# Kernel tuning notes

Hardware: AMD Instinct MI355X
Metric: run time of the kernel (lower is better)

## Reference

```python
import jax, jax.numpy as jnp
import numpy as np

EPS = 1e-6


def setup_inputs() -> dict:
    key = jax.random.key(0)
    T, B, D, n, K = 2048, 16, 1024, 64, 3
    k0, k1, k2 = jax.random.split(key, 3)
    x = jax.random.normal(k0, (T, B, D), dtype=jnp.float32)
    # xavier-ish scale for projections
    scale = 1.0 / np.sqrt(D).astype(np.float32)
    W_kv = jax.random.normal(k1, (K * 2 * n, D), dtype=jnp.float32) * scale
    W_q = jax.random.normal(k2, (n, D), dtype=jnp.float32) * scale
    B_gates = jnp.full((K, n), 2.0, dtype=jnp.float32)  # init.constant_(B_gates, 2.0)
    M_init = jnp.zeros((K, B, n, n), dtype=jnp.float32)
    return {"x": x, "M_init": M_init, "W_kv": W_kv, "W_q": W_q, "B_gates": B_gates}


def reference(x, M_init, W_kv, W_q, B_gates):
    # x: [T, B, D]; M_init: [K, B, n, n]; W_kv: [K*2*n, D]; W_q: [n, D]; B_gates: [K, n]
    T, B, D = x.shape
    K, n = B_gates.shape
    # fused kv projection, interleaved per level: [T, B, K, 2, n]
    kv = jnp.einsum('tbd,pd->tbp', x, W_kv).reshape(T, B, K, 2, n)
    k_all = jnp.transpose(kv[:, :, :, 0, :], (0, 2, 1, 3))  # [T, K, B, n]
    v_all = jnp.transpose(kv[:, :, :, 1, :], (0, 2, 1, 3))  # [T, K, B, n]
    q_all = jnp.einsum('tbd,nd->tbn', x, W_q)                # [T, B, n]
    b = B_gates[:, None, :]                                  # [K, 1, n] broadcast over batch

    def step(M, inputs):
        # M: [K, B, n, n]
        k_t, v_t, q_t = inputs
        k_norm = k_t / (jnp.linalg.norm(k_t, axis=-1, keepdims=True) + EPS)  # [K,B,n]
        gater = jnp.roll(M, shift=-1, axis=0)  # gater for level i is M[(i+1) % K]
        row_gate = jax.nn.sigmoid(jnp.einsum('kbij,kbj->kbi', gater, k_norm) + b)
        col_gate = jax.nn.sigmoid(jnp.einsum('kbji,kbj->kbi', gater, k_norm) + b)
        retrieved = jnp.einsum('kbij,kbj->kbi', M, k_norm)
        delta = v_t - retrieved
        M_new = (row_gate[..., None] * M * col_gate[:, :, None, :]
                 + jnp.einsum('kbi,kbj->kbij', delta, k_norm))
        Sq = jnp.einsum('bij,bj->bi', M_new[0], q_t)  # query against tower 0
        out = Sq * jax.nn.sigmoid(Sq)                  # self-gated output (SiLU self-gate)
        return M_new, out

    M_final, outputs = jax.lax.scan(step, M_init, (k_all, v_all, q_all))
    return outputs, M_final  # [T, B, n], [K, B, n, n]
```

## Files before the change

kernel.cpp:

```cpp
#include <hip/hip_runtime.h>
#include <hip/hip_bf16.h>
#include <math.h>

#define TT 2048
#define BB_ 16
#define DD 1024
#define NN 64
#define KK 3
#define PP 448

typedef float  v2f  __attribute__((ext_vector_type(2)));
typedef float  f4   __attribute__((ext_vector_type(4)));
typedef float  f32x4 __attribute__((ext_vector_type(4)));
typedef short  bh8  __attribute__((ext_vector_type(8)));

__device__ __forceinline__ float sigmoidf_(float x) {
    return 1.0f / (1.0f + __expf(-x));
}

#define LDS_BARRIER() __asm__ volatile("s_waitcnt lgkmcnt(0)\n\ts_barrier" ::: "memory")

template<int CTRL>
__device__ __forceinline__ float dpp_mov(float v) {
    int r = __builtin_amdgcn_update_dpp(0, __float_as_int(v), CTRL, 0xF, 0xF, true);
    return __int_as_float(r);
}

__device__ __forceinline__ float sel16_dpp(const float v[4], int s) {
    const int s0 = s & 1, s1 = (s >> 1) & 1;
    float k0 = s0 ? v[1] : v[0], d0 = s0 ? v[0] : v[1];
    float k1 = s0 ? v[3] : v[2], d1 = s0 ? v[2] : v[3];
    float a0 = k0 + dpp_mov<0xB1>(d0);
    float a1 = k1 + dpp_mov<0xB1>(d1);
    float kb = s1 ? a1 : a0, db = s1 ? a0 : a1;
    float r  = kb + dpp_mov<0x4E>(db);
    r += dpp_mov<0x124>(r);
    r += dpp_mov<0x128>(r);
    return r;
}

__global__ __launch_bounds__(256) void cvt_w_kernel(
    const float* __restrict__ Wkv,
    const float* __restrict__ Wq,
    unsigned short* __restrict__ Wsw)
{
    const int n = blockIdx.x;
    const int tid = threadIdx.x;
    const float* row = (n < 384) ? (Wkv + (size_t)n * DD)
                                 : (Wq  + (size_t)(n - 384) * DD);
    const int idx = tid * 4;
    const int kb = idx >> 5, kk = idx & 31;
    float4 f = *(const float4*)(row + idx);
    __hip_bfloat162 h0 = __float22bfloat162_rn(make_float2(f.x, f.y));
    __hip_bfloat162 h1 = __float22bfloat162_rn(make_float2(f.z, f.w));
    unsigned u0, u1;
    __builtin_memcpy(&u0, &h0, 4);
    __builtin_memcpy(&u1, &h1, 4);
    ushort4 o = make_ushort4((unsigned short)u0, (unsigned short)(u0 >> 16),
                             (unsigned short)u1, (unsigned short)(u1 >> 16));
    *(ushort4*)&Wsw[((size_t)kb * PP + n) * 32 + kk] = o;
}

__global__ __launch_bounds__(256) void mfma_proj_kernel(
    const float* __restrict__ x,
    const unsigned short* __restrict__ Wsw,
    float* __restrict__ kvq)
{
    const int tid  = threadIdx.x;
    const int w    = tid >> 6;
    const int lane = tid & 63;
    const int ln   = lane & 15;
    const int quad = lane >> 4;
    const int m0   = blockIdx.x * 64;

    f32x4 acc[28];
    #pragma unroll
    for (int t = 0; t < 28; ++t) acc[t] = (f32x4){0.f, 0.f, 0.f, 0.f};

    const float* xrow = x + (size_t)(m0 + 16 * w + ln) * DD + quad * 8;

    for (int kb = 0; kb < 32; ++kb) {
        float4 a0 = *(const float4*)(xrow + kb * 32);
        float4 a1 = *(const float4*)(xrow + kb * 32 + 4);
        __hip_bfloat162 h0 = __float22bfloat162_rn(make_float2(a0.x, a0.y));
        __hip_bfloat162 h1 = __float22bfloat162_rn(make_float2(a0.z, a0.w));
        __hip_bfloat162 h2 = __float22bfloat162_rn(make_float2(a1.x, a1.y));
        __hip_bfloat162 h3 = __float22bfloat162_rn(make_float2(a1.z, a1.w));
        unsigned u0, u1, u2, u3;
        __builtin_memcpy(&u0, &h0, 4); __builtin_memcpy(&u1, &h1, 4);
        __builtin_memcpy(&u2, &h2, 4); __builtin_memcpy(&u3, &h3, 4);
        bh8 a;
        a[0] = (short)u0; a[1] = (short)(u0 >> 16);
        a[2] = (short)u1; a[3] = (short)(u1 >> 16);
        a[4] = (short)u2; a[5] = (short)(u2 >> 16);
        a[6] = (short)u3; a[7] = (short)(u3 >> 16);

        const unsigned short* wp_ = Wsw + (size_t)kb * PP * 32 + quad * 8;
        #pragma unroll
        for (int t = 0; t < 28; ++t) {
            const bh8 bfr = *(const bh8*)(wp_ + (16 * t + ln) * 32);
            acc[t] = __builtin_amdgcn_mfma_f32_16x16x32_bf16(a, bfr, acc[t], 0, 0, 0);
        }
    }

    #pragma unroll
    for (int g = 0; g < 3; ++g) {
        const int t0 = g * 8;
        #pragma unroll
        for (int reg = 0; reg < 4; ++reg) {
            float ss = acc[t0][reg] * acc[t0][reg]
                     + acc[t0 + 1][reg] * acc[t0 + 1][reg]
                     + acc[t0 + 2][reg] * acc[t0 + 2][reg]
                     + acc[t0 + 3][reg] * acc[t0 + 3][reg];
            #pragma unroll
            for (int m = 1; m <= 8; m <<= 1) ss += __shfl_xor(ss, m, 64);
            const float sc = 1.0f / (sqrtf(ss) + 1e-6f);
            #pragma unroll
            for (int t = t0; t < t0 + 4; ++t) acc[t][reg] *= sc;
        }
    }

    float* orow = kvq + (size_t)(m0 + 16 * w + quad * 4) * PP + ln;
    #pragma unroll
    for (int t = 0; t < 28; ++t)
        #pragma unroll
        for (int reg = 0; reg < 4; ++reg)
            orow[(size_t)reg * PP + 16 * t] = acc[t][reg];
}

__global__ __launch_bounds__(1024) void scan_kernel(
    const float* __restrict__ kvq,
    const float* __restrict__ M_init,
    const float* __restrict__ B_gates,
    float* __restrict__ d_out)
{
    const int b    = blockIdx.x;
    const int tid  = threadIdx.x;
    const int wid  = tid >> 6;
    const int lane = tid & 63;

    __shared__ __align__(16) float cs_lds[2][3][4][4][64];
    __shared__ __align__(16) float rg_lds[2][3][64];
    __shared__ __align__(16) float cg_lds[2][3][64];

    if (wid >= 12) {
        const int  act = (wid < 15);
        const int  cls = act ? (wid - 12) : 0;
        const float cbias = act ? B_gates[cls * NN + lane] : 0.f;
        #pragma unroll 2
        for (int t = 0; t < TT; ++t) {
            const int pb = t & 1;
            LDS_BARRIER();
            if (act) {
                float s0 = (cs_lds[pb][cls][0][0][lane] + cs_lds[pb][cls][0][1][lane])
                         + (cs_lds[pb][cls][0][2][lane] + cs_lds[pb][cls][0][3][lane]);
                float s1 = (cs_lds[pb][cls][1][0][lane] + cs_lds[pb][cls][1][1][lane])
                         + (cs_lds[pb][cls][1][2][lane] + cs_lds[pb][cls][1][3][lane]);
                float s2 = (cs_lds[pb][cls][2][0][lane] + cs_lds[pb][cls][2][1][lane])
                         + (cs_lds[pb][cls][2][2][lane] + cs_lds[pb][cls][2][3][lane]);
                float s3 = (cs_lds[pb][cls][3][0][lane] + cs_lds[pb][cls][3][1][lane])
                         + (cs_lds[pb][cls][3][2][lane] + cs_lds[pb][cls][3][3][lane]);
                cg_lds[pb][cls][lane] = sigmoidf_((s0 + s1) + (s2 + s3) + cbias);
            }
            LDS_BARRIER();
        }
        return;
    }

    const int k    = wid >> 2;
    const int q    = wid & 3;
    const int tr   = lane >> 4;
    const int tc   = lane & 15;
    const int kp   = (k + 2) % 3;
    const int row0 = 16 * q + 4 * tr;
    const int col0 = 4 * tc;
    const int s3   = tc & 3;
    const int rowS = row0 + s3;

    v2f M2[4][2];
    #pragma unroll
    for (int i = 0; i < 4; ++i) {
        f4 t = *(const f4*)(M_init + (((size_t)k * BB_ + b) * NN + row0 + i) * NN + col0);
        M2[i][0] = (v2f){t.x, t.y};
        M2[i][1] = (v2f){t.z, t.w};
    }

    const float bias_pub_r = B_gates[kp * NN + rowS];

    float* outp = d_out;
    float* Mout = d_out + (size_t)TT * BB_ * NN;

    const int o_knc = k * 128 + col0;
    const int o_wpc = kp * 128 + col0;
    const int o_wpr = kp * 128 + row0;
    const int o_v   = k * 128 + 64 + rowS;
    const int o_q   = 384 + col0;

    const float* kvt = kvq + (size_t)b * PP;

    f4 sK[2], sC[2], sR[2], sQ[2];
    float sV[2];
    sK[0] = *(const f4*)(kvt + o_knc);
    sC[0] = *(const f4*)(kvt + o_wpc);
    sR[0] = *(const f4*)(kvt + o_wpr);
    sV[0] = kvt[o_v];
    sQ[0] = (f4){0.f, 0.f, 0.f, 0.f};
    if (k == 0) sQ[0] = *(const f4*)(kvt + o_q);
    f4 qp = sQ[0];

    #pragma unroll 2
    for (int t = 0; t < TT; ++t) {
        const int pb  = t & 1;
        const int cur = t & 1, nxt = cur ^ 1;

        const float* kvn = (t + 1 < TT) ? (kvt + (size_t)BB_ * PP) : kvt;
        sK[nxt] = *(const f4*)(kvn + o_knc);
        sC[nxt] = *(const f4*)(kvn + o_wpc);
        sR[nxt] = *(const f4*)(kvn + o_wpr);
        sV[nxt] = kvn[o_v];
        if (k == 0) sQ[nxt] = *(const f4*)(kvn + o_q);

        v2f cp2a, cp2b;
        {
            const v2f w0 = {sR[cur].x, sR[cur].x};
            cp2a = M2[0][0] * w0;
            cp2b = M2[0][1] * w0;
        }
        #pragma unroll
        for (int i = 1; i < 4; ++i) {
            const float w = (i == 1) ? sR[cur].y : (i == 2) ? sR[cur].z : sR[cur].w;
            const v2f wv = {w, w};
            cp2a += M2[i][0] * wv;
            cp2b += M2[i][1] * wv;
        }
        *(f4*)&cs_lds[pb][kp][q][tr][col0] = (f4){cp2a.x, cp2a.y, cp2b.x, cp2b.y};
        LDS_BARRIER();

        const v2f kn2a = {sK[cur].x, sK[cur].y}, kn2b = {sK[cur].z, sK[cur].w};
        const v2f wc2a = {sC[cur].x, sC[cur].y}, wc2b = {sC[cur].z, sC[cur].w};

        v2f rp2[4], sp2[4];
        #pragma unroll
        for (int i = 0; i < 4; ++i) {
            rp2[i] = M2[i][0] * kn2a + M2[i][1] * kn2b;
            sp2[i] = M2[i][0] * wc2a + M2[i][1] * wc2b;
        }
        float rp[4], sp[4];
        #pragma unroll
        for (int i = 0; i < 4; ++i) { rp[i] = rp2[i].x + rp2[i].y; sp[i] = sp2[i].x + sp2[i].y; }

        const float rsv = sel16_dpp(sp, s3);
        const float rtv = sel16_dpp(rp, s3);
        const float dv  = sV[cur] - rtv;

        if (tc < 4)
            rg_lds[pb][kp][rowS] = sigmoidf_(rsv + bias_pub_r);
        LDS_BARRIER();

        const f4 rg4 = *(const f4*)&rg_lds[pb][k][row0];
        const f4 cg4 = *(const f4*)&cg_lds[pb][k][col0];

        const float dd0 = dpp_mov<0x00>(dv);
        const float dd1 = dpp_mov<0x55>(dv);
        const float dd2 = dpp_mov<0xAA>(dv);
        const float dd3 = dpp_mov<0xFF>(dv);

        if (k == 0) {
            const v2f qpa = {qp.x, qp.y}, qpb = {qp.z, qp.w};
            float op[4];
            #pragma unroll
            for (int i = 0; i < 4; ++i) {
                v2f o2 = M2[i][0] * qpa + M2[i][1] * qpb;
                op[i] = o2.x + o2.y;
            }
            const float ov = sel16_dpp(op, s3);
            if (t > 0 && tc < 4)
                outp[((size_t)(t - 1) * BB_ + b) * NN + rowS] = ov * sigmoidf_(ov);
        }

        const v2f cg2a = {cg4.x, cg4.y}, cg2b = {cg4.z, cg4.w};
        #pragma unroll
        for (int i = 0; i < 4; ++i) {
            const float rgi = (i == 0) ? rg4.x : (i == 1) ? rg4.y : (i == 2) ? rg4.z : rg4.w;
            const float ddi = (i == 0) ? dd0  : (i == 1) ? dd1  : (i == 2) ? dd2  : dd3;
            const v2f r2 = {rgi, rgi};
            const v2f d2 = {ddi, ddi};
            M2[i][0] = r2 * (M2[i][0] * cg2a) + d2 * kn2a;
            M2[i][1] = r2 * (M2[i][1] * cg2b) + d2 * kn2b;
        }

        qp  = sQ[cur];
        kvt = kvn;
    }

    if (k == 0) {
        const v2f qpa = {qp.x, qp.y}, qpb = {qp.z, qp.w};
        float op[4];
        #pragma unroll
        for (int i = 0; i < 4; ++i) {
            v2f o2 = M2[i][0] * qpa + M2[i][1] * qpb;
            op[i] = o2.x + o2.y;
        }
        const float ov = sel16_dpp(op, s3);
        if (tc < 4)
            outp[((size_t)(TT - 1) * BB_ + b) * NN + rowS] = ov * sigmoidf_(ov);
    }

    #pragma unroll
    for (int i = 0; i < 4; ++i) {
        f4 v = (f4){M2[i][0].x, M2[i][0].y, M2[i][1].x, M2[i][1].y};
        *(f4*)&Mout[(((size_t)k * BB_ + b) * NN + row0 + i) * NN + col0] = v;
    }
}

extern "C" void kernel_launch(void* const* d_in, const int* in_sizes, int n_in,
                              void* d_out, int out_size, void* d_ws, size_t ws_size,
                              hipStream_t stream) {
    const float* x       = (const float*)d_in[0];
    const float* M_init  = (const float*)d_in[1];
    const float* W_kv    = (const float*)d_in[2];
    const float* W_q     = (const float*)d_in[3];
    const float* B_gates = (const float*)d_in[4];
    float* out = (float*)d_out;

    float* kvq = (float*)d_ws;
    const size_t kvq_bytes = (size_t)TT * BB_ * PP * 4;
    unsigned short* Wsw = (unsigned short*)((char*)d_ws + kvq_bytes);

    cvt_w_kernel<<<PP, 256, 0, stream>>>(W_kv, W_q, Wsw);
    mfma_proj_kernel<<<TT * BB_ / 64, 256, 0, stream>>>(x, Wsw, kvq);
    scan_kernel<<<BB_, 1024, 0, stream>>>(kvq, M_init, B_gates, out);
}
```

Measured before the change: 2.088 ms.

## Retile projection GEMM so each wave owns a column slice across all rows

The bf16 MFMA projection kernel's warp tiling changes from each wave covering 16 rows by all 448 columns to each wave covering all 64 rows by a 112-column slice. Each wave now loads 4 A fragments and 7 B fragments per k-step instead of 1 and 28, so it issues far fewer global loads of the weight matrix per MFMA. The k-normalisation moves to waves 0-2, since each of those waves now holds one whole key group of 64 columns. The cost is that x rows are read and converted by every wave, and the scan kernel probably dominates total time, so the end-to-end effect may be small.

```diff
diff --git a/kernel.cpp b/kernel.cpp
--- a/kernel.cpp
+++ b/kernel.cpp
@@ -73,59 +73,76 @@
     const int quad = lane >> 4;
     const int m0   = blockIdx.x * 64;
 
-    f32x4 acc[28];
+    f32x4 acc[4][7];
     #pragma unroll
-    for (int t = 0; t < 28; ++t) acc[t] = (f32x4){0.f, 0.f, 0.f, 0.f};
-
-    const float* xrow = x + (size_t)(m0 + 16 * w + ln) * DD + quad * 8;
+    for (int g = 0; g < 4; ++g)
+        #pragma unroll
+        for (int c = 0; c < 7; ++c) acc[g][c] = (f32x4){0.f, 0.f, 0.f, 0.f};
+
+    const float* xbase = x + (size_t)(m0 + ln) * DD + quad * 8;
 
     for (int kb = 0; kb < 32; ++kb) {
-        float4 a0 = *(const float4*)(xrow + kb * 32);
-        float4 a1 = *(const float4*)(xrow + kb * 32 + 4);
-        __hip_bfloat162 h0 = __float22bfloat162_rn(make_float2(a0.x, a0.y));
-        __hip_bfloat162 h1 = __float22bfloat162_rn(make_float2(a0.z, a0.w));
-        __hip_bfloat162 h2 = __float22bfloat162_rn(make_float2(a1.x, a1.y));
-        __hip_bfloat162 h3 = __float22bfloat162_rn(make_float2(a1.z, a1.w));
-        unsigned u0, u1, u2, u3;
-        __builtin_memcpy(&u0, &h0, 4); __builtin_memcpy(&u1, &h1, 4);
-        __builtin_memcpy(&u2, &h2, 4); __builtin_memcpy(&u3, &h3, 4);
-        bh8 a;
-        a[0] = (short)u0; a[1] = (short)(u0 >> 16);
-        a[2] = (short)u1; a[3] = (short)(u1 >> 16);
-        a[4] = (short)u2; a[5] = (short)(u2 >> 16);
-        a[6] = (short)u3; a[7] = (short)(u3 >> 16);
-
-        const unsigned short* wp_ = Wsw + (size_t)kb * PP * 32 + quad * 8;
-        #pragma unroll
-        for (int t = 0; t < 28; ++t) {
-            const bh8 bfr = *(const bh8*)(wp_ + (16 * t + ln) * 32);
-            acc[t] = __builtin_amdgcn_mfma_f32_16x16x32_bf16(a, bfr, acc[t], 0, 0, 0);
+        bh8 a[4];
+        #pragma unroll
+        for (int g = 0; g < 4; ++g) {
+            const float* xr = xbase + (size_t)(16 * g) * DD + kb * 32;
+            float4 a0 = *(const float4*)(xr);
+            float4 a1 = *(const float4*)(xr + 4);
+            __hip_bfloat162 h0 = __float22bfloat162_rn(make_float2(a0.x, a0.y));
+            __hip_bfloat162 h1 = __float22bfloat162_rn(make_float2(a0.z, a0.w));
+            __hip_bfloat162 h2 = __float22bfloat162_rn(make_float2(a1.x, a1.y));
+            __hip_bfloat162 h3 = __float22bfloat162_rn(make_float2(a1.z, a1.w));
+            unsigned u0, u1, u2, u3;
+            __builtin_memcpy(&u0, &h0, 4); __builtin_memcpy(&u1, &h1, 4);
+            __builtin_memcpy(&u2, &h2, 4); __builtin_memcpy(&u3, &h3, 4);
+            a[g][0] = (short)u0; a[g][1] = (short)(u0 >> 16);
+            a[g][2] = (short)u1; a[g][3] = (short)(u1 >> 16);
+            a[g][4] = (short)u2; a[g][5] = (short)(u2 >> 16);
+            a[g][6] = (short)u3; a[g][7] = (short)(u3 >> 16);
+        }
+
+        const unsigned short* wp_ = Wsw + (size_t)kb * PP * 32
+                                  + (size_t)(w * 112 + ln) * 32 + quad * 8;
+        bh8 bf[7];
+        #pragma unroll
+        for (int c = 0; c < 7; ++c)
+            bf[c] = *(const bh8*)(wp_ + (size_t)c * 16 * 32);
+
+        #pragma unroll
+        for (int c = 0; c < 7; ++c)
+            #pragma unroll
+            for (int g = 0; g < 4; ++g)
+                acc[g][c] = __builtin_amdgcn_mfma_f32_16x16x32_bf16(a[g], bf[c], acc[g][c], 0, 0, 0);
+    }
+
+    if (w < 3) {
+        const int off = w;
+        #pragma unroll
+        for (int g = 0; g < 4; ++g) {
+            #pragma unroll
+            for (int reg = 0; reg < 4; ++reg) {
+                float ss = acc[g][off][reg] * acc[g][off][reg]
+                         + acc[g][off + 1][reg] * acc[g][off + 1][reg]
+                         + acc[g][off + 2][reg] * acc[g][off + 2][reg]
+                         + acc[g][off + 3][reg] * acc[g][off + 3][reg];
+                #pragma unroll
+                for (int m = 1; m <= 8; m <<= 1) ss += __shfl_xor(ss, m, 64);
+                const float sc = 1.0f / (sqrtf(ss) + 1e-6f);
+                #pragma unroll
+                for (int c = off; c < off + 4; ++c) acc[g][c][reg] *= sc;
+            }
         }
     }
 
     #pragma unroll
-    for (int g = 0; g < 3; ++g) {
-        const int t0 = g * 8;
-        #pragma unroll
-        for (int reg = 0; reg < 4; ++reg) {
-            float ss = acc[t0][reg] * acc[t0][reg]
-                     + acc[t0 + 1][reg] * acc[t0 + 1][reg]
-                     + acc[t0 + 2][reg] * acc[t0 + 2][reg]
-                     + acc[t0 + 3][reg] * acc[t0 + 3][reg];
+    for (int g = 0; g < 4; ++g) {
+        float* orow = kvq + (size_t)(m0 + 16 * g + quad * 4) * PP + w * 112 + ln;
+        #pragma unroll
+        for (int c = 0; c < 7; ++c)
             #pragma unroll
-            for (int m = 1; m <= 8; m <<= 1) ss += __shfl_xor(ss, m, 64);
-            const float sc = 1.0f / (sqrtf(ss) + 1e-6f);
-            #pragma unroll
-            for (int t = t0; t < t0 + 4; ++t) acc[t][reg] *= sc;
-        }
-    }
-
-    float* orow = kvq + (size_t)(m0 + 16 * w + quad * 4) * PP + ln;
-    #pragma unroll
-    for (int t = 0; t < 28; ++t)
-        #pragma unroll
-        for (int reg = 0; reg < 4; ++reg)
-            orow[(size_t)reg * PP + 16 * t] = acc[t][reg];
+            for (int reg = 0; reg < 4; ++reg)
+                orow[(size_t)reg * PP + 16 * c] = acc[g][c][reg];
+    }
 }
 
 __global__ __launch_bounds__(1024) void scan_kernel(
```

Result: no change. 2.102 ms (+0.7%).
